# Kernel optimization log

Hardware: AMD Instinct MI355X
Metric: run time of the kernel (lower is better)

The kernel has to match this reference:

```python
import jax, jax.numpy as jnp
import numpy as np

B, T, NSEL, NCLS = 16, 30, 5, 10  # batch, frames/clip, top-k frames, eval classes


def _conv(x, w, s):
    # NCHW conv, SAME padding (matches Conv2d(k=3, stride=s, padding=1))
    return jax.lax.conv_general_dilated(
        x, w, (s, s), 'SAME', dimension_numbers=('NCHW', 'OIHW', 'NCHW'))


def setup_inputs() -> dict:
    key = jax.random.key(0)
    ks = jax.random.split(key, 10)
    return {
        'Full_Frame64': jax.random.uniform(ks[0], (B, T, 3, 64, 64), jnp.float32),
        'Full_Frame224': jax.random.uniform(ks[1], (B, T, 3, 224, 224), jnp.float32),
        'skim_w1': jax.random.normal(ks[2], (32, 3, 3, 3), jnp.float32) * 0.05,
        'skim_w2': jax.random.normal(ks[3], (64, 32, 3, 3), jnp.float32) * 0.05,
        'pol_w': jax.random.normal(ks[4], (64, T), jnp.float32) * 0.05,
        'pol_b': jnp.zeros((T,), jnp.float32),
        'eval_w1': jax.random.normal(ks[5], (64, 3, 3, 3), jnp.float32) * 0.05,
        'eval_w2': jax.random.normal(ks[6], (128, 64, 3, 3), jnp.float32) * 0.05,
        'eval_fc_w': jax.random.normal(ks[7], (128, NCLS), jnp.float32) * 0.05,
        'eval_fc_b': jnp.zeros((NCLS,), jnp.float32),
    }


def reference(Full_Frame64, Full_Frame224, skim_w1, skim_w2, pol_w, pol_b,
              eval_w1, eval_w2, eval_fc_w, eval_fc_b):
    # --- skim branch: concat 30 frames along H, bilinear resize to 64x64 ---
    cat64 = Full_Frame64.transpose(0, 2, 1, 3, 4).reshape(B, 3, T * 64, 64)
    skim_in = jax.vmap(lambda im: jax.image.resize(im, (3, 64, 64), 'bilinear'))(cat64)
    h = jax.nn.relu(_conv(skim_in, skim_w1, 2))
    h = jax.nn.relu(_conv(h, skim_w2, 2))
    fea = h.mean((2, 3))  # [B, 64]
    # PolicyNet: nn.ReLU(nn.Linear(...)) bug => the inner Linear(64,64) is skipped
    logits = jax.nn.relu(fea) @ pol_w + pol_b          # [B, 30]
    dist = jax.lax.stop_gradient(jax.nn.softmax(logits, axis=1))  # detached in torch
    # --- per-sample top-5 frame selection, indices sorted ascending ---
    _, idx = jax.lax.top_k(dist, NSEL)
    idx = jnp.sort(idx, axis=1)                        # [B, 5]
    # --- gather selected 224-frames, concat along H, resize to 224x224 ---
    sel = jnp.take_along_axis(Full_Frame224, idx[:, :, None, None, None], axis=1)
    cat224 = sel.transpose(0, 2, 1, 3, 4).reshape(B, 3, NSEL * 224, 224)
    eval_in = jax.vmap(lambda im: jax.image.resize(im, (3, 224, 224), 'bilinear'))(cat224)
    g = jax.nn.relu(_conv(eval_in, eval_w1, 2))
    g = jax.nn.relu(_conv(g, eval_w2, 2))
    out = g.mean((2, 3)) @ eval_fc_w + eval_fc_b       # [B, NCLS]
    return out
```

## Files before the change

### kernel.cpp

```cpp
#include <hip/hip_runtime.h>

#define BB 16
#define TT 30
#define NSEL 5
#define NCLS 10

typedef __attribute__((ext_vector_type(8))) short short8_t;
typedef __attribute__((ext_vector_type(4))) float f32x4;

__device__ inline unsigned short f2bf(float x) {
    unsigned int u = __float_as_uint(x);
    unsigned int r = u + 0x7FFFu + ((u >> 16) & 1u);
    return (unsigned short)(r >> 16);
}

__global__ __launch_bounds__(256) void prep_all(const float* __restrict__ ff64,
                                                const float* __restrict__ w2,
                                                const float* __restrict__ w1,
                                                float* __restrict__ skim_res,
                                                unsigned short* __restrict__ wpk,
                                                unsigned short* __restrict__ wpk1,
                                                float* __restrict__ gsum,
                                                float* __restrict__ gsum2) {
    int bid = blockIdx.x;
    int t = threadIdx.x;
    if (bid < 192) {
        int gid = bid * 256 + t;
        int xg = gid & 15;
        int oy = (gid >> 4) & 63;
        int bc = gid >> 10;
        int c = bc % 3, b = bc / 3;
        int ox0 = xg * 4;
        float sample = 30.f * (float)oy + 14.5f;
        int jlo = max(0, 30 * oy - 16);
        int jhi = min(TT * 64 - 1, 30 * oy + 45);
        float ax = 0.f, ay = 0.f, az = 0.f, aw = 0.f, ws = 0.f;
        for (int j = jlo; j <= jhi; ++j) {
            float w = fmaxf(0.f, 1.f - fabsf(sample - (float)j) * (1.f / 30.f));
            int tt = j >> 6, y = j & 63;
            const float4 v = *(const float4*)&ff64[(((b * TT + tt) * 3 + c) << 12) + (y << 6) + ox0];
            ax += w * v.x; ay += w * v.y; az += w * v.z; aw += w * v.w;
            ws += w;
        }
        float inv = 1.f / ws;
        float4 r; r.x = ax * inv; r.y = ay * inv; r.z = az * inv; r.w = aw * inv;
        *(float4*)&skim_res[(((b * 3 + c) << 6) + oy) * 64 + ox0] = r;
    } else {
        int i = (bid - 192) * 256 + t;
        if (i < BB * 128) gsum[i] = 0.f;
        if (i < BB * 64) gsum2[i] = 0.f;
        if (i < 4 * 64 * 8) {
            int j = i & 7;
            int lane = (i >> 3) & 63;
            int af = i >> 9;
            int oc = af * 16 + (lane & 15);
            int k = ((lane >> 4) << 3) + j;
            wpk1[i] = (k < 27) ? f2bf(w1[oc * 27 + k]) : (unsigned short)0;
        }
        if (i < 9 * 2 * 8 * 64 * 8) {
            int j = i & 7;
            int lane = (i >> 3) & 63;
            int af = (i >> 9) & 7;
            int h = (i >> 12) & 1;
            int tap = i >> 13;
            int oc = af * 16 + (lane & 15);
            int ic = h * 32 + ((lane >> 4) << 3) + j;
            int ky = tap / 3, kx = tap % 3;
            wpk[i] = f2bf(w2[((size_t)(oc * 64 + ic)) * 9 + ky * 3 + kx]);
        }
    }
}

__global__ __launch_bounds__(256) void sconv_fused(const float* __restrict__ skim_res,
                                                   const float* __restrict__ w1,
                                                   const float* __restrict__ w2,
                                                   float* __restrict__ gsum2) {
    int oy = blockIdx.x;
    int ocg = blockIdx.y;
    int b = blockIdx.z;
    int t = threadIdx.x;
    int oc = t & 31;
    int oxg = t >> 5;

    __shared__ float sr_s[3][7][64];
    __shared__ float w1_s[27][32];
    __shared__ float in_s[32][3][32];
    __shared__ float w_s[288 * 32];

    int ry0 = oy * 4;
    for (int u = t; u < 3 * 7 * 64; u += 256) {
        int ix = u & 63;
        int ry = (u >> 6) % 7;
        int ch = u / 448;
        int row = ry0 + ry;
        sr_s[ch][ry][ix] = (row < 64) ? skim_res[(((b * 3 + ch) << 6) + row) * 64 + ix] : 0.f;
    }
    for (int u = t; u < 864; u += 256) {
        int o = u & 31;
        int k = u >> 5;
        w1_s[k][o] = w1[o * 27 + k];
    }
    for (int u = t; u < 9216; u += 256) {
        int ocl = u / 288;
        int rem = u - ocl * 288;
        w_s[rem * 32 + (ocl ^ (rem & 31))] = w2[(ocg * 32 + ocl) * 288 + rem];
    }
    __syncthreads();

    for (int u = t; u < 32 * 3 * 32; u += 256) {
        int ix = u & 31;
        int ry = (u >> 5) % 3;
        int o1 = u / 96;
        int iy1 = 2 * oy + ry;
        float v = 0.f;
        if (iy1 < 32) {
            float acc = 0.f;
            #pragma unroll
            for (int ch = 0; ch < 3; ++ch) {
                #pragma unroll
                for (int ky = 0; ky < 3; ++ky) {
                    int lr = 2 * ry + ky;
                    #pragma unroll
                    for (int kx = 0; kx < 3; ++kx) {
                        int col = 2 * ix + kx;
                        float x = (col < 64) ? sr_s[ch][lr][col] : 0.f;
                        acc += w1_s[ch * 9 + ky * 3 + kx][o1] * x;
                    }
                }
            }
            v = fmaxf(acc, 0.f);
        }
        in_s[o1][ry][ix] = v;
    }
    __syncthreads();

    float acc0 = 0.f, acc1 = 0.f;
    for (int ic = 0; ic < 32; ++ic) {
        #pragma unroll
        for (int ky = 0; ky < 3; ++ky) {
            float xv[5];
            #pragma unroll
            for (int i = 0; i < 5; ++i) {
                int ix = oxg * 4 + i;
                xv[i] = (ix < 32) ? in_s[ic][ky][ix] : 0.f;
            }
            #pragma unroll
            for (int kx = 0; kx < 3; ++kx) {
                int R = ic * 9 + ky * 3 + kx;
                float wv = w_s[R * 32 + (oc ^ (R & 31))];
                acc0 += wv * xv[kx];
                acc1 += wv * xv[2 + kx];
            }
        }
    }
    float ps = fmaxf(acc0, 0.f) + fmaxf(acc1, 0.f);
    ps += __shfl_xor(ps, 32);
    if ((t & 32) == 0) atomicAdd(&gsum2[b * 64 + ocg * 32 + oc], ps);
}

__global__ __launch_bounds__(256) void conv1_fused(const float* __restrict__ ff224,
                                                   const float* __restrict__ gsum2,
                                                   const float* __restrict__ pol_w,
                                                   const float* __restrict__ pol_b,
                                                   const unsigned short* __restrict__ wpk1,
                                                   unsigned short* __restrict__ outcl) {
    int oxT = blockIdx.x;
    int oyT = blockIdx.y;
    int b = blockIdx.z;
    int t = threadIdx.x;
    int w = t >> 6;
    int lane = t & 63;
    int col = lane & 15;
    int kq = lane >> 4;

    __shared__ float fea[64];
    __shared__ float logits[TT];
    __shared__ unsigned char insel[TT];
    __shared__ int sidx[NSEL];
    __shared__ unsigned short in_s[3][9][36];

    if (t < 64) fea[t] = fmaxf(gsum2[b * 64 + t] * (1.f / 256.f), 0.f);
    __syncthreads();
    if (t < TT) {
        float l = pol_b[t];
        for (int cc = 0; cc < 64; ++cc) l += fea[cc] * pol_w[cc * TT + t];
        logits[t] = l;
    }
    __syncthreads();
    if (t < TT) {
        float li = logits[t];
        int rank = 0;
        for (int j = 0; j < TT; ++j) {
            float lj = logits[j];
            rank += (lj > li) || (lj == li && j < t);
        }
        insel[t] = (rank < NSEL) ? 1 : 0;
    }
    __syncthreads();
    if (t < TT && insel[t]) {
        int pos = 0;
        for (int j = 0; j < t; ++j) pos += insel[j];
        sidx[pos] = t;
    }
    __syncthreads();

    int iy0 = oyT * 8, ix0 = oxT * 32;
    if (t < 243) {
        int rx0 = (t % 9) * 4;
        int ry = (t / 9) % 9;
        int ic = t / 81;
        int oy = iy0 + ry;
        int ox0 = ix0 + rx0;
        ushort4 v4 = {0, 0, 0, 0};
        if (oy < 224 && ox0 < 224) {
            float sample = 5.f * (float)oy + 2.f;
            int j0 = 5 * oy - 3;
            float ax = 0.f, ay = 0.f, az = 0.f, aw = 0.f, wsum = 0.f;
            #pragma unroll
            for (int dj = 0; dj < 11; ++dj) {
                int j = j0 + dj;
                float wt = (j >= 0 && j < NSEL * 224)
                               ? fmaxf(0.f, 1.f - fabsf(sample - (float)j) * 0.2f) : 0.f;
                int jc = min(max(j, 0), NSEL * 224 - 1);
                int s = jc / 224, y = jc % 224;
                int tf = sidx[s];
                const float4 v = *(const float4*)&ff224[((size_t)((b * TT + tf) * 3 + ic) * 224 + y) * 224 + ox0];
                ax += wt * v.x; ay += wt * v.y; az += wt * v.z; aw += wt * v.w;
                wsum += wt;
            }
            float inv = 1.f / wsum;
            v4.x = f2bf(ax * inv); v4.y = f2bf(ay * inv);
            v4.z = f2bf(az * inv); v4.w = f2bf(aw * inv);
        }
        *(ushort4*)&in_s[ic][ry][rx0] = v4;
    }
    __syncthreads();

    short8_t a[4];
    #pragma unroll
    for (int af = 0; af < 4; ++af)
        a[af] = *(const short8_t*)&wpk1[((af << 6) + lane) << 3];

    unsigned int bw[4];
    #pragma unroll
    for (int jj = 0; jj < 4; ++jj) {
        unsigned int lo = 0, hi = 0;
        int k0 = (kq << 3) + jj * 2;
        {
            int k = k0;
            if (k < 27) {
                int ic = k / 9, r9 = k - ic * 9;
                int ky = r9 / 3, kx = r9 - ky * 3;
                lo = in_s[ic][2 * w + ky][2 * col + kx];
            }
        }
        {
            int k = k0 + 1;
            if (k < 27) {
                int ic = k / 9, r9 = k - ic * 9;
                int ky = r9 / 3, kx = r9 - ky * 3;
                hi = in_s[ic][2 * w + ky][2 * col + kx];
            }
        }
        bw[jj] = lo | (hi << 16);
    }
    short8_t bv;
    {
        unsigned int* bvp = (unsigned int*)&bv;
        bvp[0] = bw[0]; bvp[1] = bw[1]; bvp[2] = bw[2]; bvp[3] = bw[3];
    }

    f32x4 acc[4];
    #pragma unroll
    for (int af = 0; af < 4; ++af) {
        acc[af] = (f32x4){0.f, 0.f, 0.f, 0.f};
        acc[af] = __builtin_amdgcn_mfma_f32_16x16x32_bf16(a[af], bv, acc[af], 0, 0, 0);
    }

    int oy = oyT * 4 + w;
    int ox = oxT * 16 + col;
    size_t pxb = ((size_t)((b * 112 + oy) * 112 + ox)) << 6;
    #pragma unroll
    for (int af = 0; af < 4; ++af) {
        unsigned int p0 = f2bf(fmaxf(acc[af][0], 0.f)) | ((unsigned int)f2bf(fmaxf(acc[af][1], 0.f)) << 16);
        unsigned int p1 = f2bf(fmaxf(acc[af][2], 0.f)) | ((unsigned int)f2bf(fmaxf(acc[af][3], 0.f)) << 16);
        uint2 pk; pk.x = p0; pk.y = p1;
        *(uint2*)&outcl[pxb + (af << 4) + (kq << 2)] = pk;
    }
}

__global__ __launch_bounds__(256) void conv2_mfma(const unsigned short* __restrict__ g1cl,
                                                  const unsigned short* __restrict__ wpk,
                                                  float* __restrict__ gsum) {
    int oyT = blockIdx.x;
    int oxT = blockIdx.y;
    int b = blockIdx.z;
    int t = threadIdx.x;
    int wv = t >> 6;
    int lane = t & 63;
    int col = lane & 15;
    int kq = lane >> 4;

    __shared__ unsigned short tile[9 * 34 * 64];

    int iy0 = oyT * 8, ix0 = oxT * 32;
    for (int u = t; u < 9 * 34 * 8; u += 256) {
        int cg = u & 7;
        int r = u >> 3;
        int rx = r % 34, ry = r / 34;
        int iy = iy0 + ry, ix = ix0 + rx;
        uint4 v = {0, 0, 0, 0};
        if (iy < 112 && ix < 112)
            v = *(const uint4*)&g1cl[(((size_t)((b * 112 + iy) * 112 + ix)) << 6) + (cg << 3)];
        int byte = ((r << 6) + (cg << 3)) << 1;
        byte ^= ((r >> 1) & 7) << 4;
        *(uint4*)((char*)tile + byte) = v;
    }
    __syncthreads();

    f32x4 acc[2][4];
    #pragma unroll
    for (int a = 0; a < 2; ++a)
        #pragma unroll
        for (int n = 0; n < 4; ++n)
            acc[a][n] = (f32x4){0.f, 0.f, 0.f, 0.f};

    #pragma unroll 1
    for (int tap = 0; tap < 9; ++tap) {
        const int ky = tap / 3;
        const int kx = tap - ky * 3;
        const int rxl = 2 * col + kx;
        #pragma unroll
        for (int h = 0; h < 2; ++h) {
            const unsigned short* wp = wpk + ((size_t)(((tap * 2 + h) * 8) + (wv << 1)) * 64 + lane) * 8;
            short8_t a0 = *(const short8_t*)wp;
            short8_t a1 = *(const short8_t*)(wp + 512);
            const int e = (h << 5) + (kq << 3);
            #pragma unroll
            for (int nf = 0; nf < 4; ++nf) {
                int r = (2 * nf + ky) * 34 + rxl;
                int byte = (((r << 6) + e) << 1) ^ (((r >> 1) & 7) << 4);
                short8_t bv = *(const short8_t*)((const char*)tile + byte);
                acc[0][nf] = __builtin_amdgcn_mfma_f32_16x16x32_bf16(a0, bv, acc[0][nf], 0, 0, 0);
                acc[1][nf] = __builtin_amdgcn_mfma_f32_16x16x32_bf16(a1, bv, acc[1][nf], 0, 0, 0);
            }
        }
    }

    #pragma unroll
    for (int a = 0; a < 2; ++a) {
        float s0 = 0.f, s1 = 0.f, s2 = 0.f, s3 = 0.f;
        #pragma unroll
        for (int nf = 0; nf < 4; ++nf) {
            s0 += fmaxf(acc[a][nf][0], 0.f);
            s1 += fmaxf(acc[a][nf][1], 0.f);
            s2 += fmaxf(acc[a][nf][2], 0.f);
            s3 += fmaxf(acc[a][nf][3], 0.f);
        }
        #pragma unroll
        for (int off = 1; off < 16; off <<= 1) {
            s0 += __shfl_xor(s0, off);
            s1 += __shfl_xor(s1, off);
            s2 += __shfl_xor(s2, off);
            s3 += __shfl_xor(s3, off);
        }
        if (col == 0) {
            int ocb = wv * 32 + a * 16 + kq * 4;
            atomicAdd(&gsum[b * 128 + ocb + 0], s0);
            atomicAdd(&gsum[b * 128 + ocb + 1], s1);
            atomicAdd(&gsum[b * 128 + ocb + 2], s2);
            atomicAdd(&gsum[b * 128 + ocb + 3], s3);
        }
    }
}

__global__ void fc_kernel(const float* __restrict__ gsum, const float* __restrict__ fcw,
                          const float* __restrict__ fcb, float* __restrict__ out) {
    int gid = blockIdx.x * blockDim.x + threadIdx.x;
    if (gid >= BB * NCLS) return;
    int cls = gid % NCLS, b = gid / NCLS;
    float s = 0.f;
    for (int c = 0; c < 128; ++c) s += gsum[b * 128 + c] * fcw[c * NCLS + cls];
    out[gid] = fcb[cls] + s * (1.f / 3136.f);
}

extern "C" void kernel_launch(void* const* d_in, const int* in_sizes, int n_in,
                              void* d_out, int out_size, void* d_ws, size_t ws_size,
                              hipStream_t stream) {
    const float* ff64  = (const float*)d_in[0];
    const float* ff224 = (const float*)d_in[1];
    const float* sw1   = (const float*)d_in[2];
    const float* sw2   = (const float*)d_in[3];
    const float* polw  = (const float*)d_in[4];
    const float* polb  = (const float*)d_in[5];
    const float* ew1   = (const float*)d_in[6];
    const float* ew2   = (const float*)d_in[7];
    const float* fcw   = (const float*)d_in[8];
    const float* fcb   = (const float*)d_in[9];
    float* out = (float*)d_out;

    float* ws = (float*)d_ws;
    float* skim_res = ws;
    float* gsum2 = skim_res + 196608;
    float* gsum = gsum2 + 1024;
    unsigned short* g1cl = (unsigned short*)(gsum + 2048);
    unsigned short* wpk  = g1cl + 12845056;
    unsigned short* wpk1 = wpk + 73728;

    prep_all<<<480, 256, 0, stream>>>(ff64, ew2, ew1, skim_res, wpk, wpk1, gsum, gsum2);

    sconv_fused<<<dim3(16, 2, BB), 256, 0, stream>>>(skim_res, sw1, sw2, gsum2);

    conv1_fused<<<dim3(7, 28, BB), 256, 0, stream>>>(ff224, gsum2, polw, polb, wpk1, g1cl);

    conv2_mfma<<<dim3(14, 4, BB), 256, 0, stream>>>(g1cl, wpk, gsum);

    fc_kernel<<<1, 256, 0, stream>>>(gsum, fcw, fcb, out);
}
```

Before: 105.4 us.

## Fuse eval conv1 into conv2 kernel, computing conv1 tile with halo in LDS

Merges the resize+conv1 kernel into the conv2 MFMA kernel. Each block now resizes a 19x72 input region, computes the conv1 output tile with halo (9x34 pixels, 64 channels) directly into swizzled LDS, then runs conv2 from there. This removes the global write and read of the 112x112x64 bf16 intermediate and one kernel launch. In exchange it recomputes the halo rows and columns and adds the policy/top-k prologue to fewer, larger blocks, which also reduces the grid size and parallelism.

```diff
diff --git a/kernel.cpp b/kernel.cpp
--- a/kernel.cpp
+++ b/kernel.cpp
@@ -158,14 +158,15 @@
     if ((t & 32) == 0) atomicAdd(&gsum2[b * 64 + ocg * 32 + oc], ps);
 }
 
-__global__ __launch_bounds__(256) void conv1_fused(const float* __restrict__ ff224,
-                                                   const float* __restrict__ gsum2,
-                                                   const float* __restrict__ pol_w,
-                                                   const float* __restrict__ pol_b,
-                                                   const unsigned short* __restrict__ wpk1,
-                                                   unsigned short* __restrict__ outcl) {
-    int oxT = blockIdx.x;
-    int oyT = blockIdx.y;
+__global__ __launch_bounds__(256) void eval_fused(const float* __restrict__ ff224,
+                                                  const float* __restrict__ gsum2,
+                                                  const float* __restrict__ pol_w,
+                                                  const float* __restrict__ pol_b,
+                                                  const unsigned short* __restrict__ wpk1,
+                                                  const unsigned short* __restrict__ wpk,
+                                                  float* __restrict__ gsum) {
+    int oyT = blockIdx.x;
+    int oxT = blockIdx.y;
     int b = blockIdx.z;
     int t = threadIdx.x;
     int w = t >> 6;
@@ -177,7 +178,8 @@
     __shared__ float logits[TT];
     __shared__ unsigned char insel[TT];
     __shared__ int sidx[NSEL];
-    __shared__ unsigned short in_s[3][9][36];
+    __shared__ unsigned short res_s[3][19][72];
+    __shared__ unsigned short tile[9 * 34 * 64];
 
     if (t < 64) fea[t] = fmaxf(gsum2[b * 64 + t] * (1.f / 256.f), 0.f);
     __syncthreads();
@@ -204,17 +206,17 @@
     }
     __syncthreads();
 
-    int iy0 = oyT * 8, ix0 = oxT * 32;
-    if (t < 243) {
-        int rx0 = (t % 9) * 4;
-        int ry = (t / 9) % 9;
-        int ic = t / 81;
-        int oy = iy0 + ry;
-        int ox0 = ix0 + rx0;
+    int r0 = oyT * 16;
+    int c0 = oxT * 64;
+    for (int u = t; u < 1026; u += 256) {
+        int g = u % 18; int tmp = u / 18;
+        int rr = tmp % 19; int ch = tmp / 19;
+        int row = r0 + rr;
+        int cb = c0 + g * 4;
         ushort4 v4 = {0, 0, 0, 0};
-        if (oy < 224 && ox0 < 224) {
-            float sample = 5.f * (float)oy + 2.f;
-            int j0 = 5 * oy - 3;
+        if (row < 224 && cb + 3 < 224) {
+            float sample = 5.f * (float)row + 2.f;
+            int j0 = 5 * row - 3;
             float ax = 0.f, ay = 0.f, az = 0.f, aw = 0.f, wsum = 0.f;
             #pragma unroll
             for (int dj = 0; dj < 11; ++dj) {
@@ -224,7 +226,7 @@
                 int jc = min(max(j, 0), NSEL * 224 - 1);
                 int s = jc / 224, y = jc % 224;
                 int tf = sidx[s];
-                const float4 v = *(const float4*)&ff224[((size_t)((b * TT + tf) * 3 + ic) * 224 + y) * 224 + ox0];
+                const float4 v = *(const float4*)&ff224[((size_t)((b * TT + tf) * 3 + ch) * 224 + y) * 224 + cb];
                 ax += wt * v.x; ay += wt * v.y; az += wt * v.z; aw += wt * v.w;
                 wsum += wt;
             }
@@ -232,92 +234,81 @@
             v4.x = f2bf(ax * inv); v4.y = f2bf(ay * inv);
             v4.z = f2bf(az * inv); v4.w = f2bf(aw * inv);
         }
-        *(ushort4*)&in_s[ic][ry][rx0] = v4;
-    }
-    __syncthreads();
-
-    short8_t a[4];
-    #pragma unroll
-    for (int af = 0; af < 4; ++af)
-        a[af] = *(const short8_t*)&wpk1[((af << 6) + lane) << 3];
-
-    unsigned int bw[4];
-    #pragma unroll
-    for (int jj = 0; jj < 4; ++jj) {
-        unsigned int lo = 0, hi = 0;
-        int k0 = (kq << 3) + jj * 2;
-        {
-            int k = k0;
-            if (k < 27) {
-                int ic = k / 9, r9 = k - ic * 9;
-                int ky = r9 / 3, kx = r9 - ky * 3;
-                lo = in_s[ic][2 * w + ky][2 * col + kx];
-            }
-        }
-        {
-            int k = k0 + 1;
-            if (k < 27) {
-                int ic = k / 9, r9 = k - ic * 9;
-                int ky = r9 / 3, kx = r9 - ky * 3;
-                hi = in_s[ic][2 * w + ky][2 * col + kx];
-            }
-        }
-        bw[jj] = lo | (hi << 16);
-    }
-    short8_t bv;
+        *(ushort4*)&res_s[ch][rr][g * 4] = v4;
+    }
+    __syncthreads();
+
+    int iy0 = oyT * 8, ix0 = oxT * 32;
     {
-        unsigned int* bvp = (unsigned int*)&bv;
-        bvp[0] = bw[0]; bvp[1] = bw[1]; bvp[2] = bw[2]; bvp[3] = bw[3];
-    }
-
-    f32x4 acc[4];
-    #pragma unroll
-    for (int af = 0; af < 4; ++af) {
-        acc[af] = (f32x4){0.f, 0.f, 0.f, 0.f};
-        acc[af] = __builtin_amdgcn_mfma_f32_16x16x32_bf16(a[af], bv, acc[af], 0, 0, 0);
-    }
-
-    int oy = oyT * 4 + w;
-    int ox = oxT * 16 + col;
-    size_t pxb = ((size_t)((b * 112 + oy) * 112 + ox)) << 6;
-    #pragma unroll
-    for (int af = 0; af < 4; ++af) {
-        unsigned int p0 = f2bf(fmaxf(acc[af][0], 0.f)) | ((unsigned int)f2bf(fmaxf(acc[af][1], 0.f)) << 16);
-        unsigned int p1 = f2bf(fmaxf(acc[af][2], 0.f)) | ((unsigned int)f2bf(fmaxf(acc[af][3], 0.f)) << 16);
-        uint2 pk; pk.x = p0; pk.y = p1;
-        *(uint2*)&outcl[pxb + (af << 4) + (kq << 2)] = pk;
-    }
-}
-
-__global__ __launch_bounds__(256) void conv2_mfma(const unsigned short* __restrict__ g1cl,
-                                                  const unsigned short* __restrict__ wpk,
-                                                  float* __restrict__ gsum) {
-    int oyT = blockIdx.x;
-    int oxT = blockIdx.y;
-    int b = blockIdx.z;
-    int t = threadIdx.x;
-    int wv = t >> 6;
-    int lane = t & 63;
-    int col = lane & 15;
-    int kq = lane >> 4;
-
-    __shared__ unsigned short tile[9 * 34 * 64];
-
-    int iy0 = oyT * 8, ix0 = oxT * 32;
-    for (int u = t; u < 9 * 34 * 8; u += 256) {
-        int cg = u & 7;
-        int r = u >> 3;
-        int rx = r % 34, ry = r / 34;
-        int iy = iy0 + ry, ix = ix0 + rx;
-        uint4 v = {0, 0, 0, 0};
-        if (iy < 112 && ix < 112)
-            v = *(const uint4*)&g1cl[(((size_t)((b * 112 + iy) * 112 + ix)) << 6) + (cg << 3)];
-        int byte = ((r << 6) + (cg << 3)) << 1;
-        byte ^= ((r >> 1) & 7) << 4;
-        *(uint4*)((char*)tile + byte) = v;
-    }
-    __syncthreads();
-
+        short8_t a1f[4];
+        #pragma unroll
+        for (int af = 0; af < 4; ++af)
+            a1f[af] = *(const short8_t*)&wpk1[((af << 6) + lane) << 3];
+
+        #pragma unroll 1
+        for (int g = w * 5; g < w * 5 + 5; ++g) {
+            int px = g * 16 + col;
+            int pxc = min(px, 305);
+            int r = pxc / 34;
+            int c = pxc - r * 34;
+
+            unsigned int bw[4];
+            #pragma unroll
+            for (int jj = 0; jj < 4; ++jj) {
+                unsigned int lo = 0, hi = 0;
+                int k0 = (kq << 3) + jj * 2;
+                {
+                    int k = k0;
+                    if (k < 27) {
+                        int ic = k / 9, r9 = k - ic * 9;
+                        int ky = r9 / 3, kx = r9 - ky * 3;
+                        lo = res_s[ic][2 * r + ky][2 * c + kx];
+                    }
+                }
+                {
+                    int k = k0 + 1;
+                    if (k < 27) {
+                        int ic = k / 9, r9 = k - ic * 9;
+                        int ky = r9 / 3, kx = r9 - ky * 3;
+                        hi = res_s[ic][2 * r + ky][2 * c + kx];
+                    }
+                }
+                bw[jj] = lo | (hi << 16);
+            }
+            short8_t bv;
+            {
+                unsigned int* bvp = (unsigned int*)&bv;
+                bvp[0] = bw[0]; bvp[1] = bw[1]; bvp[2] = bw[2]; bvp[3] = bw[3];
+            }
+
+            f32x4 a4[4];
+            #pragma unroll
+            for (int af = 0; af < 4; ++af) {
+                a4[af] = (f32x4){0.f, 0.f, 0.f, 0.f};
+                a4[af] = __builtin_amdgcn_mfma_f32_16x16x32_bf16(a1f[af], bv, a4[af], 0, 0, 0);
+            }
+
+            if (px < 306) {
+                bool ok = (iy0 + r < 112) && (ix0 + c < 112);
+                #pragma unroll
+                for (int af = 0; af < 4; ++af) {
+                    uint2 pk;
+                    if (ok) {
+                        pk.x = f2bf(fmaxf(a4[af][0], 0.f)) | ((unsigned int)f2bf(fmaxf(a4[af][1], 0.f)) << 16);
+                        pk.y = f2bf(fmaxf(a4[af][2], 0.f)) | ((unsigned int)f2bf(fmaxf(a4[af][3], 0.f)) << 16);
+                    } else {
+                        pk.x = 0; pk.y = 0;
+                    }
+                    int oc0 = (af << 4) + (kq << 2);
+                    int byte = (((px << 6) + oc0) << 1) ^ (((px >> 1) & 7) << 4);
+                    *(uint2*)((char*)tile + byte) = pk;
+                }
+            }
+        }
+    }
+    __syncthreads();
+
+    int wv = w;
     f32x4 acc[2][4];
     #pragma unroll
     for (int a = 0; a < 2; ++a)
@@ -403,17 +394,14 @@
     float* skim_res = ws;
     float* gsum2 = skim_res + 196608;
     float* gsum = gsum2 + 1024;
-    unsigned short* g1cl = (unsigned short*)(gsum + 2048);
-    unsigned short* wpk  = g1cl + 12845056;
+    unsigned short* wpk  = (unsigned short*)(gsum + 2048);
     unsigned short* wpk1 = wpk + 73728;
 
     prep_all<<<480, 256, 0, stream>>>(ff64, ew2, ew1, skim_res, wpk, wpk1, gsum, gsum2);
 
     sconv_fused<<<dim3(16, 2, BB), 256, 0, stream>>>(skim_res, sw1, sw2, gsum2);
 
-    conv1_fused<<<dim3(7, 28, BB), 256, 0, stream>>>(ff224, gsum2, polw, polb, wpk1, g1cl);
-
-    conv2_mfma<<<dim3(14, 4, BB), 256, 0, stream>>>(g1cl, wpk, gsum);
+    eval_fused<<<dim3(14, 4, BB), 256, 0, stream>>>(ff224, gsum2, polw, polb, wpk1, wpk, gsum);
 
     fc_kernel<<<1, 256, 0, stream>>>(gsum, fcw, fcb, out);
 }
```

Measured after the change: 97.02 us. 1.09x faster.
